# Optimization experiments

Hardware: AMD Instinct MI355X
Metric: run time of the kernel (lower is better)

Reference implementation:

```python
import jax, jax.numpy as jnp
import numpy as np
from jax import lax

B, T, IN = 32, 512, 32
SNN, TS, HID, HOR = 128, 4, 128, 96
K = 3
THR = 1.0
EPS = 1e-5


def _spike(x):
    # heaviside: fires when (mem - threshold) > 0
    return (x > 0).astype(x.dtype)


def _lif_scan(xs, beta, thr):
    """snntorch Leaky (reset_mechanism='subtract'): mem_t = beta*mem_{t-1} + x_t - spk_{t-1}*thr; spk_t = H(mem_t - thr).
    xs: (S, B, C); beta: (C,). Returns spikes (S,B,C) and membrane (S,B,C)."""
    def step(carry, x):
        mem, rst = carry
        mem = beta * mem + x - rst * thr
        spk = _spike(mem - thr)
        return (mem, lax.stop_gradient(spk)), (spk, mem)
    z = jnp.zeros(xs.shape[1:], xs.dtype)
    _, (spks, mems) = lax.scan(step, (z, z), xs)
    return spks, mems


def setup_inputs() -> dict:
    key = jax.random.key(0)
    ks = jax.random.split(key, 10)
    def rn(k, shape, scale=0.05):
        return jax.random.normal(k, shape, dtype=jnp.float32) * scale
    return {
        "x": jax.random.normal(ks[0], (B, T, IN), dtype=jnp.float32),
        "conv_w": rn(ks[1], (SNN * TS, IN, K)),
        "conv_b": jnp.zeros((SNN * TS,), jnp.float32),
        "bn1_g": jnp.ones((SNN * TS,), jnp.float32),
        "bn1_b": jnp.zeros((SNN * TS,), jnp.float32),
        "beta1": jnp.full((SNN,), 0.9, jnp.float32),
        "bn2_g": jnp.ones((SNN,), jnp.float32),
        "bn2_b": jnp.zeros((SNN,), jnp.float32),
        "beta2": jnp.full((SNN,), 0.9, jnp.float32),
        "gru_wih": rn(ks[2], (3 * HID, IN + SNN)),
        "gru_whh": rn(ks[3], (3 * HID, HID)),
        "gru_bih": jnp.zeros((3 * HID,), jnp.float32),
        "gru_bhh": jnp.zeros((3 * HID,), jnp.float32),
        "q_w": rn(ks[4], (HID, HID)), "q_b": jnp.zeros((HID,), jnp.float32),
        "k_w": rn(ks[5], (HID, HID)), "k_b": jnp.zeros((HID,), jnp.float32),
        "v_w": rn(ks[6], (HID, HID)), "v_b": jnp.zeros((HID,), jnp.float32),
        "bn3_g": jnp.ones((HID,), jnp.float32),
        "bn3_b": jnp.zeros((HID,), jnp.float32),
        "head_w": rn(ks[7], (HOR, HID)),
        "head_b": jnp.zeros((HOR,), jnp.float32),
    }


def reference(x, conv_w, conv_b, bn1_g, bn1_b, beta1, bn2_g, bn2_b, beta2,
              gru_wih, gru_whh, gru_bih, gru_bhh, q_w, q_b, k_w, k_b, v_w, v_b,
              bn3_g, bn3_b, head_w, head_b):
    beta1 = jnp.clip(beta1, 0.0, 0.99)
    beta2 = jnp.clip(beta2, 0.0, 0.99)
    # --- ConvSpikeEncoder: Conv1d -> BatchNorm1d (training stats) -> LIF scan ---
    h = lax.conv_general_dilated(x.transpose(0, 2, 1), conv_w, (1,), [(K // 2, K // 2)],
                                 dimension_numbers=('NCH', 'OIH', 'NCH'))
    h = h + conv_b[None, :, None]  # (B, SNN*TS, T)
    m = h.mean((0, 2), keepdims=True)
    v = jnp.var(h, (0, 2), keepdims=True)
    h = (h - m) * lax.rsqrt(v + EPS) * bn1_g[None, :, None] + bn1_b[None, :, None]
    # (B, SNN*TS, T) -> (T*TS, B, SNN), step index = t*TS + s
    h = h.transpose(0, 2, 1).reshape(B, T * TS, SNN).transpose(1, 0, 2)
    spk_enc, _ = _lif_scan(h, beta1, THR)  # (T*TS, B, SNN)
    # --- per-step BatchNorm1d over batch dim, then second LIF ---
    m2 = spk_enc.mean(1, keepdims=True)
    v2 = jnp.var(spk_enc, 1, keepdims=True)
    h2 = (spk_enc - m2) * lax.rsqrt(v2 + EPS) * bn2_g + bn2_b
    _, mem_rec = _lif_scan(h2, beta2, THR)  # (T*TS, B, SNN)
    # --- downsample membrane: mean over TS sub-steps ---
    mem_down = mem_rec.transpose(1, 0, 2).reshape(B, T, TS, SNN).mean(2)  # (B, T, SNN)
    hc = jnp.concatenate([x, mem_down], -1)  # (B, T, IN+SNN)
    # --- GRU (PyTorch gate order r,z,n) ---
    def gstep(hprev, xt):
        gi = xt @ gru_wih.T + gru_bih
        gh = hprev @ gru_whh.T + gru_bhh
        ir, iz, inn = jnp.split(gi, 3, -1)
        hr, hz, hn = jnp.split(gh, 3, -1)
        r = jax.nn.sigmoid(ir + hr)
        zg = jax.nn.sigmoid(iz + hz)
        n = jnp.tanh(inn + r * hn)
        hnew = (1.0 - zg) * n + zg * hprev
        return hnew, hnew
    _, gru_seq = lax.scan(gstep, jnp.zeros((B, HID), x.dtype), hc.transpose(1, 0, 2))
    g = gru_seq.transpose(1, 0, 2)  # (B, T, HID)
    # --- SpikingAttention: sigmoid(QK^T*scale) @ V, mean over T, BatchNorm ---
    Q = g @ q_w.T + q_b
    Kk = g @ k_w.T + k_b
    V = g @ v_w.T + v_b
    attn = jax.nn.sigmoid(jnp.einsum('btc,bsc->bts', Q, Kk) * (HID ** -0.5))
    out = jnp.einsum('bts,bsc->btc', attn, V).mean(1)  # (B, HID)
    m3 = out.mean(0, keepdims=True)
    v3 = jnp.var(out, 0, keepdims=True)
    out = (out - m3) * lax.rsqrt(v3 + EPS) * bn3_g + bn3_b
    return out @ head_w.T + head_b  # (B, HOR)
```

## Files before the change

### kernel.cpp

```cpp
#include <hip/hip_runtime.h>
#include <math.h>

#define EPSV 1e-5f

#if __has_builtin(__builtin_amdgcn_exp2f)
#define EXP2F(x) __builtin_amdgcn_exp2f(x)
#else
#define EXP2F(x) exp2f(x)
#endif
#if __has_builtin(__builtin_amdgcn_rcpf)
#define RCPF(x) __builtin_amdgcn_rcpf(x)
#else
#define RCPF(x) (1.0f/(x))
#endif

__device__ __forceinline__ float fsigmoid(float x){
  return RCPF(1.0f + EXP2F(-1.4426950408889634f * x));
}
__device__ __forceinline__ float ftanh(float x){
  return RCPF(0.5f + 0.5f * EXP2F(-2.8853900817779268f * x)) - 1.0f;
}
__device__ __forceinline__ unsigned short f2bf(float f){
  unsigned u = __float_as_uint(f);
  return (unsigned short)((u + 0x7FFFu + ((u >> 16) & 1u)) >> 16);
}
__device__ __forceinline__ float bf2f(unsigned short u){
  return __uint_as_float(((unsigned)u) << 16);
}

typedef __attribute__((ext_vector_type(8))) short bf16x8;
typedef __attribute__((ext_vector_type(4))) float f32x4;
typedef __attribute__((ext_vector_type(2))) _Float16 f16x2;
typedef __attribute__((ext_vector_type(8))) _Float16 f16x8;

#if __has_builtin(__builtin_amdgcn_fdot2)
#define FDOT2(a,b,c) __builtin_amdgcn_fdot2(a,b,c,false)
#else
__device__ __forceinline__ float FDOT2(f16x2 a, f16x2 b, float c){
  return c + (float)a[0]*(float)b[0] + (float)a[1]*(float)b[1];
}
#endif

__device__ __forceinline__ float dot8(f16x8 w, f16x8 h, float acc){
  f16x2 w0 = {w[0],w[1]}, w1 = {w[2],w[3]}, w2 = {w[4],w[5]}, w3 = {w[6],w[7]};
  f16x2 h0 = {h[0],h[1]}, h1 = {h[2],h[3]}, h2 = {h[4],h[5]}, h3 = {h[6],h[7]};
  acc = FDOT2(w0,h0,acc); acc = FDOT2(w1,h1,acc);
  acc = FDOT2(w2,h2,acc); acc = FDOT2(w3,h3,acc);
  return acc;
}

__global__ __launch_bounds__(256) void k_convcvt(const float* __restrict__ x, const float* __restrict__ w,
        const float* __restrict__ cb, float* __restrict__ hp, float* __restrict__ s1g,
        float* __restrict__ s2g, unsigned short* __restrict__ x_bf,
        const float* __restrict__ wih, const float* __restrict__ qw, const float* __restrict__ kw,
        const float* __restrict__ vw, const float* __restrict__ whh,
        unsigned short* __restrict__ wih_bf, unsigned short* __restrict__ wqkv_bf,
        _Float16* __restrict__ whh_h){
  const int tid = threadIdx.x;
  if (blockIdx.x >= 1024){
    int i = (blockIdx.x - 1024)*256 + tid;
    if (i < 61440){ wih_bf[i] = f2bf(wih[i]); return; }
    int r = i - 61440;
    if (r < 16384){ wqkv_bf[r] = f2bf(qw[r]); return; }
    r -= 16384;
    if (r < 16384){ wqkv_bf[16384 + r] = f2bf(kw[r]); return; }
    r -= 16384;
    if (r < 16384){ wqkv_bf[32768 + r] = f2bf(vw[r]); return; }
    r -= 16384;
    if (r < 49152){ whh_h[r] = (_Float16)whh[r]; }
    return;
  }
  __shared__ float xs[32*321];
  __shared__ float ws[32*97];
  __shared__ float bs[32];
  const int t0 = (blockIdx.x >> 4) * 8;
  const int n0 = (blockIdx.x & 15) * 8;
  for (int idx = tid; idx < 32*10*32; idx += 256){
    int bq = idx / 320; int rem = idx - bq*320; int tt = rem >> 5; int i = rem & 31;
    int tg = t0 - 1 + tt;
    float v = 0.f;
    if (tg >= 0 && tg < 512) v = x[(bq*512 + tg)*32 + i];
    xs[bq*321 + tt*32 + i] = v;
  }
  for (int idx = tid; idx < 32*96; idx += 256){
    int row = idx / 96; int within = idx - row*96;
    int ss = row >> 3; int nl = row & 7;
    int c = ss*128 + n0 + nl;
    ws[row*97 + within] = w[c*96 + within];
  }
  if (tid < 32){
    int ss = tid >> 3, nl = tid & 7;
    bs[tid] = cb[ss*128 + n0 + nl];
  }
  __syncthreads();
  if ((blockIdx.x & 15) == 0){
    for (int idx = tid; idx < 32*8*32; idx += 256){
      int bq = idx >> 8; int rem = idx & 255; int tt = rem >> 5; int i = rem & 31;
      x_bf[(bq*512 + t0 + tt)*32 + i] = f2bf(xs[bq*321 + (tt+1)*32 + i]);
    }
  }
  const int b = tid & 31;
  const int nl = tid >> 5;
  float acc[4][8];
  #pragma unroll
  for (int ss = 0; ss < 4; ++ss){
    float bv = bs[ss*8 + nl];
    #pragma unroll
    for (int t = 0; t < 8; ++t) acc[ss][t] = bv;
  }
  for (int i = 0; i < 32; ++i){
    #pragma unroll
    for (int k = 0; k < 3; ++k){
      float w0 = ws[(0*8+nl)*97 + i*3 + k];
      float w1 = ws[(1*8+nl)*97 + i*3 + k];
      float w2 = ws[(2*8+nl)*97 + i*3 + k];
      float w3 = ws[(3*8+nl)*97 + i*3 + k];
      #pragma unroll
      for (int t = 0; t < 8; ++t){
        float xv = xs[b*321 + (t+k)*32 + i];
        acc[0][t] += xv*w0; acc[1][t] += xv*w1; acc[2][t] += xv*w2; acc[3][t] += xv*w3;
      }
    }
  }
  #pragma unroll
  for (int ss = 0; ss < 4; ++ss){
    int n = n0 + nl;
    float s1 = 0.f, s2 = 0.f;
    #pragma unroll
    for (int t = 0; t < 8; ++t){
      float v = acc[ss][t];
      int s = (t0 + t)*4 + ss;
      hp[s*4096 + n*32 + b] = v;
      s1 += v; s2 += v*v;
    }
    #pragma unroll
    for (int off = 1; off < 32; off <<= 1){
      s1 += __shfl_xor(s1, off);
      s2 += __shfl_xor(s2, off);
    }
    if (b == 0){
      int c = ss*128 + n;
      atomicAdd(&s1g[c], s1);
      atomicAdd(&s2g[c], s2);
    }
  }
}

__global__ __launch_bounds__(64) void k_lif(const float* __restrict__ hp,
        const float* __restrict__ s1g, const float* __restrict__ s2g,
        const float* __restrict__ g1v, const float* __restrict__ b1v,
        const float* __restrict__ beta1, const float* __restrict__ g2v, const float* __restrict__ b2v,
        const float* __restrict__ beta2, unsigned short* __restrict__ md_t){
  const int tid = threadIdx.x;
  const int b = tid & 31;
  const int n = blockIdx.x * 2 + (tid >> 5);
  float a1r[4], b1r[4];
  #pragma unroll
  for (int ss = 0; ss < 4; ++ss){
    int c = ss*128 + n;
    float m = s1g[c] * (1.f/16384.f);
    float v = s2g[c] * (1.f/16384.f) - m*m;
    float sc = g1v[c] * rsqrtf(v + EPSV);
    a1r[ss] = sc;
    b1r[ss] = b1v[c] - m*sc;
  }
  float be1 = fminf(fmaxf(beta1[n], 0.f), 0.99f);
  float be2 = fminf(fmaxf(beta2[n], 0.f), 0.99f);
  float g2 = g2v[n], bb2 = b2v[n];
  float m1 = 0.f, r1 = 0.f, m2 = 0.f, r2 = 0.f;
  const float* base = hp + n*32 + b;
  float c0 = base[0], c1 = base[4096], c2 = base[2*4096], c3 = base[3*4096];
  const float* p1 = base + 16384;
  float d0 = p1[0], d1 = p1[4096], d2 = p1[2*4096], d3 = p1[3*4096];
  const float* p2 = base + 2*16384;
  float e0 = p2[0], e1 = p2[4096], e2 = p2[2*4096], e3 = p2[3*4096];

#define LIF_STEP(CV, A1R, B1R) { \
    float x1 = CV*A1R + B1R; \
    m1 = be1*m1 + x1 - r1; \
    bool sp = (m1 > 1.0f); \
    unsigned long long mk = __ballot(sp); \
    float spk = sp ? 1.f : 0.f; r1 = spk; \
    unsigned hf = (tid & 32) ? (unsigned)(mk >> 32) : (unsigned)mk; \
    float mean = (float)__popc(hf) * 0.03125f; \
    float var = mean - mean*mean; \
    float h2 = (spk - mean) * rsqrtf(var + EPSV) * g2 + bb2; \
    m2 = be2*m2 + h2 - r2; \
    r2 = (m2 > 1.0f) ? 1.f : 0.f; \
    accd += m2; }

  for (int t = 0; t < 512; ++t){
    float f0 = 0.f, f1 = 0.f, f2 = 0.f, f3 = 0.f;
    if (t < 509){
      const float* nb = base + (size_t)(t+3)*16384;
      f0 = nb[0]; f1 = nb[4096]; f2 = nb[2*4096]; f3 = nb[3*4096];
    }
    float accd = 0.f;
    LIF_STEP(c0, a1r[0], b1r[0])
    LIF_STEP(c1, a1r[1], b1r[1])
    LIF_STEP(c2, a1r[2], b1r[2])
    LIF_STEP(c3, a1r[3], b1r[3])
    md_t[((t*128) + n)*32 + b] = f2bf(accd * 0.25f);
    c0 = d0; c1 = d1; c2 = d2; c3 = d3;
    d0 = e0; d1 = e1; d2 = e2; d3 = e3;
    e0 = f0; e1 = f1; e2 = f2; e3 = f3;
  }
#undef LIF_STEP
}

__global__ __launch_bounds__(256) void k_mm_gi(const unsigned short* __restrict__ xbf,
        const unsigned short* __restrict__ md_t, const unsigned short* __restrict__ wihbf,
        const float* __restrict__ bih, unsigned short* __restrict__ gi2b){
  const int tid = threadIdx.x;
  const int w = tid >> 6, l = tid & 63;
  const int c16 = l & 15, kg = l >> 4;
  const int m0 = (blockIdx.x*4 + w) * 16;
  const int mrow = m0 + c16;
  const int bb = mrow >> 9, tt = mrow & 511;
  bf16x8 a0 = *(const bf16x8*)&xbf[(size_t)mrow*32 + kg*8];
  const unsigned short* mt = md_t + (size_t)tt*4096 + bb;
  unsigned short tmp[4][8];
  #pragma unroll
  for (int f = 0; f < 4; ++f)
    #pragma unroll
    for (int e = 0; e < 8; ++e)
      tmp[f][e] = mt[(kg*8 + f*32 + e)*32];
  bf16x8 a1 = *(bf16x8*)tmp[0];
  bf16x8 a2 = *(bf16x8*)tmp[1];
  bf16x8 a3 = *(bf16x8*)tmp[2];
  bf16x8 a4 = *(bf16x8*)tmp[3];
  for (int nt2 = 0; nt2 < 8; ++nt2){
    int n0 = nt2*16;
    const unsigned short* wr = &wihbf[(size_t)(      n0 + c16)*160 + kg*8];
    const unsigned short* wz = &wihbf[(size_t)(128 + n0 + c16)*160 + kg*8];
    const unsigned short* wn = &wihbf[(size_t)(256 + n0 + c16)*160 + kg*8];
    f32x4 ar = {0.f,0.f,0.f,0.f}, az = {0.f,0.f,0.f,0.f}, an = {0.f,0.f,0.f,0.f};
    #pragma unroll
    for (int c = 0; c < 5; ++c){
      bf16x8 br = *(const bf16x8*)(wr + c*32);
      bf16x8 bz = *(const bf16x8*)(wz + c*32);
      bf16x8 bn = *(const bf16x8*)(wn + c*32);
      bf16x8 aa = (c == 0) ? a0 : (c == 1) ? a1 : (c == 2) ? a2 : (c == 3) ? a3 : a4;
      ar = __builtin_amdgcn_mfma_f32_16x16x32_bf16(aa, br, ar, 0, 0, 0);
      az = __builtin_amdgcn_mfma_f32_16x16x32_bf16(aa, bz, az, 0, 0, 0);
      an = __builtin_amdgcn_mfma_f32_16x16x32_bf16(aa, bn, an, 0, 0, 0);
    }
    float br_ = bih[n0 + c16], bz_ = bih[128 + n0 + c16], bn_ = bih[256 + n0 + c16];
    int jj = n0 + c16;
    #pragma unroll
    for (int r = 0; r < 4; ++r){
      ushort4 o = { f2bf(ar[r] + br_), f2bf(az[r] + bz_), f2bf(an[r] + bn_), 0 };
      *(ushort4*)&gi2b[(size_t)(m0 + kg*4 + r)*512 + jj*4] = o;
    }
  }
}

template<int SEL>
__device__ __forceinline__ float dpp_qp(float x){
  return __int_as_float(__builtin_amdgcn_mov_dpp(__float_as_int(x), SEL, 0xF, 0xF, true));
}
__global__ __launch_bounds__(256, 1) void k_gru(const unsigned short* __restrict__ gi2b,
        const _Float16* __restrict__ whh_h, const float* __restrict__ bhh,
        unsigned short* __restrict__ gout_bf){
  const int b = blockIdx.x;
  const int tid = threadIdx.x;
  const int j = tid >> 1;
  const int half = tid & 1;
  const int k0 = half * 64;
  __shared__ _Float16 hs[2][144];
  const _Float16* wbr = whh_h + (size_t)(      j)*128 + k0;
  const _Float16* wbz = whh_h + (size_t)(128 + j)*128 + k0;
  const _Float16* wbn = whh_h + (size_t)(256 + j)*128 + k0;
  f16x8 wr[8], wz[8], wn[8];
  #pragma unroll
  for (int i = 0; i < 8; ++i){
    wr[i] = *(const f16x8*)(wbr + i*8);
    wz[i] = *(const f16x8*)(wbz + i*8);
    wn[i] = *(const f16x8*)(wbn + i*8);
  }
  float bh_r = 0.f, bh_z = 0.f, bh_n = 0.f;
  if (!half){
    bh_r = bhh[j]; bh_z = bhh[128+j]; bh_n = bhh[256+j];
  }
  const unsigned short* gib = gi2b + (size_t)b*512*512 + j*4;
  ushort4 G[4], N[4];
  #pragma unroll
  for (int u = 0; u < 4; ++u){
    G[u] = *(const ushort4*)(gib + (size_t)u*512);
    N[u] = *(const ushort4*)(gib + (size_t)(4+u)*512);
  }
  if (tid < 128) hs[0][tid] = (_Float16)0.f;
  float hprev = 0.f;
  __syncthreads();
  for (int g = 0; g < 128; ++g){
    ushort4 N2[4];
    if (g < 126){
      #pragma unroll
      for (int u = 0; u < 4; ++u)
        N2[u] = *(const ushort4*)(gib + (size_t)(4*(g+2)+u)*512);
    } else {
      #pragma unroll
      for (int u = 0; u < 4; ++u) N2[u] = (ushort4){0,0,0,0};
    }
    #pragma unroll
    for (int u = 0; u < 4; ++u){
      const int t = g*4 + u;
      const f16x8* hq = (const f16x8*)&hs[t & 1][k0];
      f16x8 h0 = hq[0], h1 = hq[1], h2 = hq[2], h3 = hq[3],
            h4 = hq[4], h5 = hq[5], h6 = hq[6], h7 = hq[7];
      float ar0 = 0.f, ar1 = 0.f, az0 = 0.f, az1 = 0.f, an0 = 0.f, an1 = 0.f;
      ar0 = dot8(wr[0],h0,ar0); ar0 = dot8(wr[1],h1,ar0); ar0 = dot8(wr[2],h2,ar0); ar0 = dot8(wr[3],h3,ar0);
      ar1 = dot8(wr[4],h4,ar1); ar1 = dot8(wr[5],h5,ar1); ar1 = dot8(wr[6],h6,ar1); ar1 = dot8(wr[7],h7,ar1);
      az0 = dot8(wz[0],h0,az0); az0 = dot8(wz[1],h1,az0); az0 = dot8(wz[2],h2,az0); az0 = dot8(wz[3],h3,az0);
      az1 = dot8(wz[4],h4,az1); az1 = dot8(wz[5],h5,az1); az1 = dot8(wz[6],h6,az1); az1 = dot8(wz[7],h7,az1);
      an0 = dot8(wn[0],h0,an0); an0 = dot8(wn[1],h1,an0); an0 = dot8(wn[2],h2,an0); an0 = dot8(wn[3],h3,an0);
      an1 = dot8(wn[4],h4,an1); an1 = dot8(wn[5],h5,an1); an1 = dot8(wn[6],h6,an1); an1 = dot8(wn[7],h7,an1);
      float ar = ar0 + ar1, az = az0 + az1, an = an0 + an1;
      ar += dpp_qp<0xB1>(ar);
      az += dpp_qp<0xB1>(az);
      an += dpp_qp<0xB1>(an);
      if (!half){
        float r = fsigmoid(bf2f(G[u].x) + ar + bh_r);
        float z = fsigmoid(bf2f(G[u].y) + az + bh_z);
        float nn = ftanh(bf2f(G[u].z) + r*(an + bh_n));
        float hn = (1.f - z)*nn + z*hprev;
        hprev = hn;
        hs[(t + 1) & 1][j] = (_Float16)hn;
        gout_bf[((size_t)b*512 + t)*128 + j] = f2bf(hn);
      }
      __syncthreads();
    }
    #pragma unroll
    for (int u = 0; u < 4; ++u){ G[u] = N[u]; N[u] = N2[u]; }
  }
}

__global__ __launch_bounds__(256) void k_mm_qkv(const unsigned short* __restrict__ gbf,
        const unsigned short* __restrict__ wbf, const float* __restrict__ qb2,
        const float* __restrict__ kb2, const float* __restrict__ vb2,
        unsigned short* __restrict__ Qbf, unsigned short* __restrict__ Kbf, float* __restrict__ Vb){
  const int tid = threadIdx.x;
  const int w = tid >> 6, l = tid & 63;
  const int c16 = l & 15, kg = l >> 4;
  const int m0 = (blockIdx.x*4 + w) * 16;
  const unsigned short* gp = &gbf[(size_t)(m0 + c16)*128 + kg*8];
  bf16x8 a0 = *(const bf16x8*)(gp + 0);
  bf16x8 a1 = *(const bf16x8*)(gp + 32);
  bf16x8 a2 = *(const bf16x8*)(gp + 64);
  bf16x8 a3 = *(const bf16x8*)(gp + 96);
  for (int nt = 0; nt < 24; ++nt){
    int n0 = nt*16;
    const unsigned short* wp = &wbf[(size_t)(n0 + c16)*128 + kg*8];
    bf16x8 b0 = *(const bf16x8*)(wp + 0);
    bf16x8 b1 = *(const bf16x8*)(wp + 32);
    bf16x8 b2 = *(const bf16x8*)(wp + 64);
    bf16x8 b3 = *(const bf16x8*)(wp + 96);
    f32x4 acc = {0.f,0.f,0.f,0.f};
    acc = __builtin_amdgcn_mfma_f32_16x16x32_bf16(a0, b0, acc, 0, 0, 0);
    acc = __builtin_amdgcn_mfma_f32_16x16x32_bf16(a1, b1, acc, 0, 0, 0);
    acc = __builtin_amdgcn_mfma_f32_16x16x32_bf16(a2, b2, acc, 0, 0, 0);
    acc = __builtin_amdgcn_mfma_f32_16x16x32_bf16(a3, b3, acc, 0, 0, 0);
    int n = n0 + c16;
    if (n < 128){
      float bias = qb2[n];
      #pragma unroll
      for (int r = 0; r < 4; ++r)
        Qbf[(size_t)(m0 + kg*4 + r)*128 + n] = f2bf(acc[r] + bias);
    } else if (n < 256){
      float bias = kb2[n-128];
      #pragma unroll
      for (int r = 0; r < 4; ++r)
        Kbf[(size_t)(m0 + kg*4 + r)*128 + (n-128)] = f2bf(acc[r] + bias);
    } else {
      float bias = vb2[n-256];
      #pragma unroll
      for (int r = 0; r < 4; ++r)
        Vb[(size_t)(m0 + kg*4 + r)*128 + (n-256)] = acc[r] + bias;
    }
  }
}

__global__ __launch_bounds__(256) void k_attn(const unsigned short* __restrict__ Qbf,
        const unsigned short* __restrict__ Kbf, const float* __restrict__ Vb,
        float* __restrict__ out0){
  __shared__ float avs[64];
  const int tid = threadIdx.x;
  const int b  = blockIdx.x;
  const int st = blockIdx.y;
  const int w  = tid >> 6;
  const int l  = tid & 63;
  const int c16 = l & 15;
  const int kg  = l >> 4;
  const float SC = 0.08838834764831845f;
  const unsigned short* kp = Kbf + ((size_t)(b*512 + st*64 + w*16 + c16))*128 + kg*8;
  bf16x8 a0 = *(const bf16x8*)(kp + 0);
  bf16x8 a1 = *(const bf16x8*)(kp + 32);
  bf16x8 a2 = *(const bf16x8*)(kp + 64);
  bf16x8 a3 = *(const bf16x8*)(kp + 96);
  const unsigned short* qb = Qbf + ((size_t)(b*512 + c16))*128 + kg*8;
  float ps0 = 0.f, ps1 = 0.f, ps2 = 0.f, ps3 = 0.f;
  for (int tt = 0; tt < 32; ++tt){
    const unsigned short* qp = qb + (size_t)tt*16*128;
    bf16x8 b0 = *(const bf16x8*)(qp + 0);
    bf16x8 b1 = *(const bf16x8*)(qp + 32);
    bf16x8 b2 = *(const bf16x8*)(qp + 64);
    bf16x8 b3 = *(const bf16x8*)(qp + 96);
    f32x4 acc = {0.f, 0.f, 0.f, 0.f};
    acc = __builtin_amdgcn_mfma_f32_16x16x32_bf16(a0, b0, acc, 0, 0, 0);
    acc = __builtin_amdgcn_mfma_f32_16x16x32_bf16(a1, b1, acc, 0, 0, 0);
    acc = __builtin_amdgcn_mfma_f32_16x16x32_bf16(a2, b2, acc, 0, 0, 0);
    acc = __builtin_amdgcn_mfma_f32_16x16x32_bf16(a3, b3, acc, 0, 0, 0);
    ps0 += fsigmoid(acc[0]*SC);
    ps1 += fsigmoid(acc[1]*SC);
    ps2 += fsigmoid(acc[2]*SC);
    ps3 += fsigmoid(acc[3]*SC);
  }
  #pragma unroll
  for (int off = 1; off < 16; off <<= 1){
    ps0 += __shfl_xor(ps0, off);
    ps1 += __shfl_xor(ps1, off);
    ps2 += __shfl_xor(ps2, off);
    ps3 += __shfl_xor(ps3, off);
  }
  if (c16 == 0){
    int sl = w*16 + kg*4;
    avs[sl + 0] = ps0 * (1.f/512.f);
    avs[sl + 1] = ps1 * (1.f/512.f);
    avs[sl + 2] = ps2 * (1.f/512.f);
    avs[sl + 3] = ps3 * (1.f/512.f);
  }
  __syncthreads();
  const int c = tid & 127;
  const int sh = tid >> 7;
  const float* vb = Vb + ((size_t)(b*512 + st*64 + sh*32))*128 + c;
  float acc = 0.f;
  #pragma unroll 8
  for (int sl = 0; sl < 32; ++sl)
    acc += avs[sh*32 + sl] * vb[(size_t)sl*128];
  atomicAdd(&out0[b*128 + c], acc);
}

__global__ __launch_bounds__(256) void k_final(const float* __restrict__ out0,
        const float* __restrict__ g3, const float* __restrict__ b3,
        const float* __restrict__ hw, const float* __restrict__ hb, float* __restrict__ out){
  __shared__ float on[2][132];
  const int tid = threadIdx.x;
  const int b0 = blockIdx.x * 2;
  if (tid < 128){
    int c = tid;
    float s = 0.f;
    #pragma unroll 8
    for (int bq = 0; bq < 32; ++bq) s += out0[bq*128 + c];
    float m = s * (1.f/32.f);
    float v = 0.f;
    #pragma unroll 8
    for (int bq = 0; bq < 32; ++bq){ float d = out0[bq*128 + c] - m; v += d*d; }
    v *= (1.f/32.f);
    float sc = g3[c] * rsqrtf(v + EPSV);
    float sh = b3[c] - m*sc;
    on[0][c] = out0[(b0+0)*128 + c]*sc + sh;
    on[1][c] = out0[(b0+1)*128 + c]*sc + sh;
  }
  __syncthreads();
  for (int o = tid; o < 2*96; o += 256){
    int bl = o / 96, hh = o - bl*96;
    float acc = hb[hh];
    for (int k = 0; k < 128; ++k) acc += on[bl][k] * hw[hh*128 + k];
    out[(b0 + bl)*96 + hh] = acc;
  }
}

extern "C" void kernel_launch(void* const* d_in, const int* in_sizes, int n_in,
                              void* d_out, int out_size, void* d_ws, size_t ws_size,
                              hipStream_t stream){
  const float* x      = (const float*)d_in[0];
  const float* conv_w = (const float*)d_in[1];
  const float* conv_b = (const float*)d_in[2];
  const float* bn1_g  = (const float*)d_in[3];
  const float* bn1_b  = (const float*)d_in[4];
  const float* beta1  = (const float*)d_in[5];
  const float* bn2_g  = (const float*)d_in[6];
  const float* bn2_b  = (const float*)d_in[7];
  const float* beta2  = (const float*)d_in[8];
  const float* g_wih  = (const float*)d_in[9];
  const float* g_whh  = (const float*)d_in[10];
  const float* g_bih  = (const float*)d_in[11];
  const float* g_bhh  = (const float*)d_in[12];
  const float* q_w    = (const float*)d_in[13];
  const float* q_b    = (const float*)d_in[14];
  const float* k_w    = (const float*)d_in[15];
  const float* k_b    = (const float*)d_in[16];
  const float* v_w    = (const float*)d_in[17];
  const float* v_b    = (const float*)d_in[18];
  const float* bn3_g  = (const float*)d_in[19];
  const float* bn3_b  = (const float*)d_in[20];
  const float* head_w = (const float*)d_in[21];
  const float* head_b = (const float*)d_in[22];

  char* ws = (char*)d_ws;
  float* hp            = (float*)ws;
  unsigned short* md_t = (unsigned short*)(ws + 37748736);
  unsigned short* g_bf = (unsigned short*)(ws + 37748736);
  unsigned short* x_bf = (unsigned short*)(ws + 41943040);
  unsigned short* wih_bf  = (unsigned short*)(ws + 42991616);
  unsigned short* wqkv_bf = (unsigned short*)(ws + 43114496);
  _Float16* whh_h      = (_Float16*)(ws + 43212800);
  float* s1g  = (float*)(ws + 50331648);
  float* s2g  = (float*)(ws + 50331648 + 2048);
  float* out0 = (float*)(ws + 50331648 + 4096);
  unsigned short* gi2b = (unsigned short*)ws;
  unsigned short* Qbf  = (unsigned short*)ws;
  unsigned short* Kbf  = (unsigned short*)(ws + 4194304);
  float* Vb   = (float*)(ws + 8388608);

  (void)hipMemsetAsync(ws + 50331648, 0, 20480, stream);

  k_convcvt<<<1648, 256, 0, stream>>>(x, conv_w, conv_b, hp, s1g, s2g, x_bf,
                                      g_wih, q_w, k_w, v_w, g_whh, wih_bf, wqkv_bf, whh_h);
  k_lif<<<64, 64, 0, stream>>>(hp, s1g, s2g, bn1_g, bn1_b, beta1, bn2_g, bn2_b, beta2, md_t);
  k_mm_gi<<<256, 256, 0, stream>>>(x_bf, md_t, wih_bf, g_bih, gi2b);
  k_gru<<<32, 256, 0, stream>>>(gi2b, whh_h, g_bhh, g_bf);
  k_mm_qkv<<<256, 256, 0, stream>>>(g_bf, wqkv_bf, q_b, k_b, v_b, Qbf, Kbf, Vb);
  k_attn<<<dim3(32, 8), 256, 0, stream>>>(Qbf, Kbf, Vb, out0);
  k_final<<<16, 256, 0, stream>>>(out0, bn3_g, bn3_b, head_w, head_b, (float*)d_out);
}
```

Baseline: 547.1 us.

## Split GRU recurrence dot products across four lanes and shrink LIF blocks

The GRU kernel now uses 512 threads per batch row, with four lanes per hidden unit each handling 32 of the 128 inputs. Partial sums are combined by two DPP butterfly steps. Each lane loads one timestep's gate input per group, and DPP quad broadcast hands it to lane 0. Fewer weight registers per thread and a shorter dot-product chain are meant to cut latency on the serial recurrence, in exchange for more threads meeting at each per-step barrier. The LIF kernel switches from 64-thread blocks to 32-thread blocks, one channel each, spreading the scan over 128 blocks instead of 64.

```diff
diff --git a/kernel.cpp b/kernel.cpp
--- a/kernel.cpp
+++ b/kernel.cpp
@@ -146,14 +146,14 @@
   }
 }
 
-__global__ __launch_bounds__(64) void k_lif(const float* __restrict__ hp,
+__global__ __launch_bounds__(32) void k_lif(const float* __restrict__ hp,
         const float* __restrict__ s1g, const float* __restrict__ s2g,
         const float* __restrict__ g1v, const float* __restrict__ b1v,
         const float* __restrict__ beta1, const float* __restrict__ g2v, const float* __restrict__ b2v,
         const float* __restrict__ beta2, unsigned short* __restrict__ md_t){
   const int tid = threadIdx.x;
   const int b = tid & 31;
-  const int n = blockIdx.x * 2 + (tid >> 5);
+  const int n = blockIdx.x;
   float a1r[4], b1r[4];
   #pragma unroll
   for (int ss = 0; ss < 4; ++ss){
@@ -181,8 +181,7 @@
     bool sp = (m1 > 1.0f); \
     unsigned long long mk = __ballot(sp); \
     float spk = sp ? 1.f : 0.f; r1 = spk; \
-    unsigned hf = (tid & 32) ? (unsigned)(mk >> 32) : (unsigned)mk; \
-    float mean = (float)__popc(hf) * 0.03125f; \
+    float mean = (float)__popc((unsigned)mk) * 0.03125f; \
     float var = mean - mean*mean; \
     float h2 = (spk - mean) * rsqrtf(var + EPSV) * g2 + bb2; \
     m2 = be2*m2 + h2 - r2; \
@@ -256,73 +255,69 @@
 }
 
 template<int SEL>
-__device__ __forceinline__ float dpp_qp(float x){
+__device__ __forceinline__ unsigned dpp_u(unsigned x){
+  return (unsigned)__builtin_amdgcn_mov_dpp((int)x, SEL, 0xF, 0xF, true);
+}
+__device__ __forceinline__ unsigned qbc_u(unsigned x, int u){
+  switch(u){
+    case 0: return dpp_u<0x00>(x);
+    case 1: return dpp_u<0x55>(x);
+    case 2: return dpp_u<0xAA>(x);
+    default: return dpp_u<0xFF>(x);
+  }
+}
+template<int SEL>
+__device__ __forceinline__ float dpp_f(float x){
   return __int_as_float(__builtin_amdgcn_mov_dpp(__float_as_int(x), SEL, 0xF, 0xF, true));
 }
-__global__ __launch_bounds__(256, 1) void k_gru(const unsigned short* __restrict__ gi2b,
+__global__ __launch_bounds__(512, 2) void k_gru(const unsigned short* __restrict__ gi2b,
         const _Float16* __restrict__ whh_h, const float* __restrict__ bhh,
         unsigned short* __restrict__ gout_bf){
   const int b = blockIdx.x;
   const int tid = threadIdx.x;
-  const int j = tid >> 1;
-  const int half = tid & 1;
-  const int k0 = half * 64;
+  const int j = tid >> 2;
+  const int q = tid & 3;
   __shared__ _Float16 hs[2][144];
-  const _Float16* wbr = whh_h + (size_t)(      j)*128 + k0;
-  const _Float16* wbz = whh_h + (size_t)(128 + j)*128 + k0;
-  const _Float16* wbn = whh_h + (size_t)(256 + j)*128 + k0;
-  f16x8 wr[8], wz[8], wn[8];
-  #pragma unroll
-  for (int i = 0; i < 8; ++i){
-    wr[i] = *(const f16x8*)(wbr + i*8);
-    wz[i] = *(const f16x8*)(wbz + i*8);
-    wn[i] = *(const f16x8*)(wbn + i*8);
-  }
+  const _Float16* wbr = whh_h + (size_t)(      j)*128 + q*32;
+  const _Float16* wbz = whh_h + (size_t)(128 + j)*128 + q*32;
+  const _Float16* wbn = whh_h + (size_t)(256 + j)*128 + q*32;
+  f16x8 wr0 = *(const f16x8*)(wbr+ 0), wr1 = *(const f16x8*)(wbr+ 8),
+        wr2 = *(const f16x8*)(wbr+16), wr3 = *(const f16x8*)(wbr+24);
+  f16x8 wz0 = *(const f16x8*)(wbz+ 0), wz1 = *(const f16x8*)(wbz+ 8),
+        wz2 = *(const f16x8*)(wbz+16), wz3 = *(const f16x8*)(wbz+24);
+  f16x8 wn0 = *(const f16x8*)(wbn+ 0), wn1 = *(const f16x8*)(wbn+ 8),
+        wn2 = *(const f16x8*)(wbn+16), wn3 = *(const f16x8*)(wbn+24);
   float bh_r = 0.f, bh_z = 0.f, bh_n = 0.f;
-  if (!half){
+  if (!q){
     bh_r = bhh[j]; bh_z = bhh[128+j]; bh_n = bhh[256+j];
   }
   const unsigned short* gib = gi2b + (size_t)b*512*512 + j*4;
-  ushort4 G[4], N[4];
-  #pragma unroll
-  for (int u = 0; u < 4; ++u){
-    G[u] = *(const ushort4*)(gib + (size_t)u*512);
-    N[u] = *(const ushort4*)(gib + (size_t)(4+u)*512);
-  }
+  uint2 G = *(const uint2*)(gib + (size_t)q*512);
+  uint2 N = *(const uint2*)(gib + (size_t)(4+q)*512);
   if (tid < 128) hs[0][tid] = (_Float16)0.f;
   float hprev = 0.f;
   __syncthreads();
   for (int g = 0; g < 128; ++g){
-    ushort4 N2[4];
-    if (g < 126){
-      #pragma unroll
-      for (int u = 0; u < 4; ++u)
-        N2[u] = *(const ushort4*)(gib + (size_t)(4*(g+2)+u)*512);
-    } else {
-      #pragma unroll
-      for (int u = 0; u < 4; ++u) N2[u] = (ushort4){0,0,0,0};
-    }
+    uint2 N2 = {0u, 0u};
+    if (g < 126) N2 = *(const uint2*)(gib + (size_t)(4*(g+2)+q)*512);
     #pragma unroll
     for (int u = 0; u < 4; ++u){
       const int t = g*4 + u;
-      const f16x8* hq = (const f16x8*)&hs[t & 1][k0];
-      f16x8 h0 = hq[0], h1 = hq[1], h2 = hq[2], h3 = hq[3],
-            h4 = hq[4], h5 = hq[5], h6 = hq[6], h7 = hq[7];
-      float ar0 = 0.f, ar1 = 0.f, az0 = 0.f, az1 = 0.f, an0 = 0.f, an1 = 0.f;
-      ar0 = dot8(wr[0],h0,ar0); ar0 = dot8(wr[1],h1,ar0); ar0 = dot8(wr[2],h2,ar0); ar0 = dot8(wr[3],h3,ar0);
-      ar1 = dot8(wr[4],h4,ar1); ar1 = dot8(wr[5],h5,ar1); ar1 = dot8(wr[6],h6,ar1); ar1 = dot8(wr[7],h7,ar1);
-      az0 = dot8(wz[0],h0,az0); az0 = dot8(wz[1],h1,az0); az0 = dot8(wz[2],h2,az0); az0 = dot8(wz[3],h3,az0);
-      az1 = dot8(wz[4],h4,az1); az1 = dot8(wz[5],h5,az1); az1 = dot8(wz[6],h6,az1); az1 = dot8(wz[7],h7,az1);
-      an0 = dot8(wn[0],h0,an0); an0 = dot8(wn[1],h1,an0); an0 = dot8(wn[2],h2,an0); an0 = dot8(wn[3],h3,an0);
-      an1 = dot8(wn[4],h4,an1); an1 = dot8(wn[5],h5,an1); an1 = dot8(wn[6],h6,an1); an1 = dot8(wn[7],h7,an1);
-      float ar = ar0 + ar1, az = az0 + az1, an = an0 + an1;
-      ar += dpp_qp<0xB1>(ar);
-      az += dpp_qp<0xB1>(az);
-      an += dpp_qp<0xB1>(an);
-      if (!half){
-        float r = fsigmoid(bf2f(G[u].x) + ar + bh_r);
-        float z = fsigmoid(bf2f(G[u].y) + az + bh_z);
-        float nn = ftanh(bf2f(G[u].z) + r*(an + bh_n));
+      unsigned grz = qbc_u(G.x, u);
+      unsigned gn  = qbc_u(G.y, u);
+      const f16x8* hq = (const f16x8*)&hs[t & 1][q*32];
+      f16x8 h0 = hq[0], h1 = hq[1], h2 = hq[2], h3 = hq[3];
+      float ar = 0.f, az = 0.f, an = 0.f;
+      ar = dot8(wr0,h0,ar); ar = dot8(wr1,h1,ar); ar = dot8(wr2,h2,ar); ar = dot8(wr3,h3,ar);
+      az = dot8(wz0,h0,az); az = dot8(wz1,h1,az); az = dot8(wz2,h2,az); az = dot8(wz3,h3,az);
+      an = dot8(wn0,h0,an); an = dot8(wn1,h1,an); an = dot8(wn2,h2,an); an = dot8(wn3,h3,an);
+      ar += dpp_f<0xB1>(ar); ar += dpp_f<0x4E>(ar);
+      az += dpp_f<0xB1>(az); az += dpp_f<0x4E>(az);
+      an += dpp_f<0xB1>(an); an += dpp_f<0x4E>(an);
+      if (!q){
+        float r = fsigmoid(bf2f((unsigned short)(grz & 0xFFFFu)) + ar + bh_r);
+        float z = fsigmoid(bf2f((unsigned short)(grz >> 16)) + az + bh_z);
+        float nn = ftanh(bf2f((unsigned short)(gn & 0xFFFFu)) + r*(an + bh_n));
         float hn = (1.f - z)*nn + z*hprev;
         hprev = hn;
         hs[(t + 1) & 1][j] = (_Float16)hn;
@@ -330,8 +325,7 @@
       }
       __syncthreads();
     }
-    #pragma unroll
-    for (int u = 0; u < 4; ++u){ G[u] = N[u]; N[u] = N2[u]; }
+    G = N; N = N2;
   }
 }
 
@@ -517,9 +511,9 @@
 
   k_convcvt<<<1648, 256, 0, stream>>>(x, conv_w, conv_b, hp, s1g, s2g, x_bf,
                                       g_wih, q_w, k_w, v_w, g_whh, wih_bf, wqkv_bf, whh_h);
-  k_lif<<<64, 64, 0, stream>>>(hp, s1g, s2g, bn1_g, bn1_b, beta1, bn2_g, bn2_b, beta2, md_t);
+  k_lif<<<128, 32, 0, stream>>>(hp, s1g, s2g, bn1_g, bn1_b, beta1, bn2_g, bn2_b, beta2, md_t);
   k_mm_gi<<<256, 256, 0, stream>>>(x_bf, md_t, wih_bf, g_bih, gi2b);
-  k_gru<<<32, 256, 0, stream>>>(gi2b, whh_h, g_bhh, g_bf);
+  k_gru<<<32, 512, 0, stream>>>(gi2b, whh_h, g_bhh, g_bf);
   k_mm_qkv<<<256, 256, 0, stream>>>(g_bf, wqkv_bf, q_b, k_b, v_b, Qbf, Kbf, Vb);
   k_attn<<<dim3(32, 8), 256, 0, stream>>>(Qbf, Kbf, Vb, out0);
   k_final<<<16, 256, 0, stream>>>(out0, bn3_g, bn3_b, head_w, head_b, (float*)d_out);
```

Result: slower. 690.3 us (+26.2%).
